# Optimization experiments

Measured on AMD Instinct MI355X. Metric: run time of the kernel, lower is better.

Reference implementation:

```python
import jax, jax.numpy as jnp
import numpy as np

C_EXP = 8.0  # fixed gate sharpness from the module (self.c = 8.0)

def setup_inputs() -> dict:
    key = jax.random.key(0)
    k1, k2, k3, k4 = jax.random.split(key, 4)
    B, T, D = 8, 4096, 1024
    x = jax.random.normal(k1, (B, T, D), dtype=jnp.float32)
    W_r = jax.random.normal(k2, (D, D), dtype=jnp.float32) * (1.0 / np.sqrt(D))
    W_i = jax.random.normal(k3, (D, D), dtype=jnp.float32) * (1.0 / np.sqrt(D))
    lambd = jax.random.normal(k4, (D,), dtype=jnp.float32)
    return {"x": x, "W_r": W_r, "W_i": W_i, "lambd": lambd}

def reference(x, W_r, W_i, lambd):
    # Gates (nn.Linear with bias=False: y = x @ W.T)
    r = jax.nn.sigmoid(jnp.einsum('btd,ed->bte', x, W_r))
    i = jax.nn.sigmoid(jnp.einsum('btd,ed->bte', x, W_i))
    # a = sigmoid(lambd) ** (c * r), computed stably in log space
    log_a = C_EXP * r * jax.nn.log_sigmoid(lambd)  # [B,T,D], log_a <= 0
    a = jnp.exp(log_a)
    # input-normalized injection: sqrt(1 - a^2) * (i * x)
    b = jnp.sqrt(jnp.maximum(1.0 - jnp.exp(2.0 * log_a), 0.0)) * (i * x)
    # linear recurrence h_t = a_t * h_{t-1} + b_t via associative scan over T
    def combine(c1, c2):
        a1, b1 = c1
        a2, b2 = c2
        return (a1 * a2, a2 * b1 + b2)
    _, h = jax.lax.associative_scan(combine, (a, b), axis=1)
    return h
```

## Files before the change

### kernel.cpp

```cpp
#include <hip/hip_runtime.h>
#include <hip/hip_bf16.h>
#include <cstdint>

#define B_   8
#define T_   4096
#define D_   1024
#define M_   (B_*T_)
#define K_   D_
#define N_   D_

#define TC2  64
#define NC2  (T_/TC2)

#define BM   256
#define BN   128
#define BK   64
#define NSTEP (K_/BK)

typedef __attribute__((ext_vector_type(8))) short  short8;
typedef __attribute__((ext_vector_type(4))) float  floatx4;

#define XB_OFF    0ull
#define WR_OFF    (XB_OFF + (size_t)M_*K_*2)
#define WI_OFF    (WR_OFF + (size_t)N_*K_*2)
#define LS_OFF    (WI_OFF + (size_t)N_*K_*2)
#define ASUM_OFF  (LS_OFF + (size_t)D_*4)
#define ESUM_OFF  (ASUM_OFF + (size_t)B_*NC2*D_*4)
#define WS_NEED   (ESUM_OFF + (size_t)B_*NC2*D_*4)

__device__ __forceinline__ uint32_t f2bf(float f) {
  uint32_t u = __float_as_uint(f);
  return (u + 0x7fffu + ((u >> 16) & 1u)) >> 16;
}

__device__ __forceinline__ void gload_lds16(const void* g, void* l) {
  __builtin_amdgcn_global_load_lds(
      (const __attribute__((address_space(1))) void*)g,
      (__attribute__((address_space(3))) void*)l, 16, 0, 0);
}

__global__ __launch_bounds__(256) void convert_kernel(
    const float* __restrict__ x, const float* __restrict__ wr,
    const float* __restrict__ wi, const float* __restrict__ lambd,
    uint2* __restrict__ xb, uint2* __restrict__ wrb, uint2* __restrict__ wib,
    float* __restrict__ ls) {
  int gid = blockIdx.x * 256 + threadIdx.x;
  if (gid < D_) {
    float l = lambd[gid];
    ls[gid] = fminf(l, 0.f) - log1pf(__expf(-fabsf(l)));
  }
  const int XQ = M_*K_/4;
  const int WQ = N_*K_/4;
  int stride = gridDim.x * 256;
  for (int q = gid; q < XQ + 2*WQ; q += stride) {
    const float4* src; uint2* dst; int i;
    if (q < XQ)           { src = (const float4*)x;  dst = xb;  i = q; }
    else if (q < XQ + WQ) { src = (const float4*)wr; dst = wrb; i = q - XQ; }
    else                  { src = (const float4*)wi; dst = wib; i = q - XQ - WQ; }
    float4 v = src[i];
    uint2 o;
    o.x = (f2bf(v.y) << 16) | f2bf(v.x);
    o.y = (f2bf(v.w) << 16) | f2bf(v.z);
    dst[i] = o;
  }
}

__global__ __launch_bounds__(512, 2) void dual_gemm_kernel(
    const short* __restrict__ xb, const short* __restrict__ wrb,
    const short* __restrict__ wib, const float* __restrict__ ls,
    uint32_t* __restrict__ ab, float* __restrict__ Asum,
    float* __restrict__ Esum) {
  __shared__ short lds[2 * 32768];

  const int tid  = threadIdx.x;
  const int lane = tid & 63;
  const int wv   = tid >> 6;
  const int wm   = wv >> 1;
  const int wn   = wv & 1;
  const int c16  = lane & 15;
  const int q    = lane >> 4;

  const int bm = blockIdx.x * BM;
  const int bn = blockIdx.y * BN;

  floatx4 accR[4][4], accI[4][4];
  #pragma unroll
  for (int i = 0; i < 4; ++i)
    #pragma unroll
    for (int j = 0; j < 4; ++j) {
      accR[i][j] = (floatx4){0.f,0.f,0.f,0.f};
      accI[i][j] = (floatx4){0.f,0.f,0.f,0.f};
    }

  const int srow   = lane >> 3;
  const int schunk = lane & 7;

  auto stage = [&](int buf, int k0) {
    short* dst = lds + buf * 32768;
    #pragma unroll
    for (int l = 0; l < 4; ++l) {
      int r  = wv*32 + l*8 + srow;
      int cc = schunk ^ (r & 7);
      gload_lds16(xb + (size_t)(bm + r)*K_ + k0 + cc*8,
                  dst + wv*2048 + l*512);
    }
    #pragma unroll
    for (int l = 0; l < 2; ++l) {
      int r  = wv*16 + l*8 + srow;
      int cc = schunk ^ (r & 7);
      gload_lds16(wrb + (size_t)(bn + r)*K_ + k0 + cc*8,
                  dst + 16384 + wv*1024 + l*512);
      gload_lds16(wib + (size_t)(bn + r)*K_ + k0 + cc*8,
                  dst + 24576 + wv*1024 + l*512);
    }
  };

  stage(0, 0);
  __syncthreads();

  for (int step = 0; step < NSTEP; ++step) {
    if (step + 1 < NSTEP) stage((step + 1) & 1, (step + 1) * BK);

    const short* As  = lds + (step & 1) * 32768;
    const short* Brs = As + 16384;
    const short* Bis = As + 24576;

    #pragma unroll
    for (int kk = 0; kk < BK/32; ++kk) {
      short8 af[4], brf[4], bif[4];
      #pragma unroll
      for (int f = 0; f < 4; ++f) {
        int m_loc = wm*64 + f*16 + c16;
        int cph   = (kk*4 + q) ^ (m_loc & 7);
        af[f]  = *(const short8*)(As  + m_loc*64 + cph*8);
        int n_loc = wn*64 + f*16 + c16;
        int cphn  = (kk*4 + q) ^ (n_loc & 7);
        brf[f] = *(const short8*)(Brs + n_loc*64 + cphn*8);
        bif[f] = *(const short8*)(Bis + n_loc*64 + cphn*8);
      }
      __builtin_amdgcn_s_setprio(1);
      #pragma unroll
      for (int fm = 0; fm < 4; ++fm)
        #pragma unroll
        for (int fn = 0; fn < 4; ++fn) {
          accR[fm][fn] = __builtin_amdgcn_mfma_f32_16x16x32_bf16(
              af[fm], brf[fn], accR[fm][fn], 0, 0, 0);
          accI[fm][fn] = __builtin_amdgcn_mfma_f32_16x16x32_bf16(
              af[fm], bif[fn], accI[fm][fn], 0, 0, 0);
        }
      __builtin_amdgcn_s_setprio(0);
    }
    __syncthreads();
  }

  const int b_idx = bm >> 12;
  const int c2    = ((bm & (T_-1)) >> 6) + wm;
  #pragma unroll
  for (int fn = 0; fn < 4; ++fn) {
    int col = bn + wn*64 + fn*16 + c16;
    float lsv = ls[col];
    float WA = 1.f, WE = 0.f;
    #pragma unroll
    for (int fm = 0; fm < 4; ++fm) {
      float SA = 1.f, SE = 0.f;
      #pragma unroll
      for (int j = 0; j < 4; ++j) {
        int row = bm + wm*64 + fm*16 + q*4 + j;
        float pr = accR[fm][fn][j];
        float pi = accI[fm][fn][j];
        float rg = 1.f / (1.f + __expf(-pr));
        float ig = 1.f / (1.f + __expf(-pi));
        float la = 8.f * rg * lsv;
        uint32_t xu = (uint32_t)(uint16_t)xb[(size_t)row*K_ + col];
        float xv = __uint_as_float(xu << 16);
        float a2 = __expf(2.f * la);
        float bb = sqrtf(fmaxf(1.f - a2, 0.f)) * ig * xv;
        uint32_t pk = (f2bf(bb) << 16) | f2bf(la);
        ab[(size_t)row*N_ + col] = pk;
        float av  = __expf(__uint_as_float(pk << 16));
        float bbr = __uint_as_float(pk & 0xffff0000u);
        SA *= av;
        SE = fmaf(av, SE, bbr);
      }
      #pragma unroll
      for (int s = 16; s <= 32; s <<= 1) {
        float OA = __shfl_xor(SA, s);
        float OE = __shfl_xor(SE, s);
        SE = (lane & s) ? fmaf(SA, OE, SE)
                        : fmaf(OA, SE, OE);
        SA *= OA;
      }
      WE = fmaf(SA, WE, SE);
      WA *= SA;
    }
    if (q == 0) {
      int o = (b_idx * NC2 + c2) * D_ + col;
      Asum[o] = WA;
      Esum[o] = WE;
    }
  }
}

__global__ __launch_bounds__(256) void scan_carry(
    float* __restrict__ Asum, const float* __restrict__ Esum) {
  int b = blockIdx.x >> 2;
  int d = ((blockIdx.x & 3) << 8) + threadIdx.x;
  float carry = 0.f;
  #pragma unroll 8
  for (int c = 0; c < NC2; ++c) {
    int o = (b*NC2 + c)*D_ + d;
    float A = Asum[o], E = Esum[o];
    Asum[o] = carry;
    carry = fmaf(A, carry, E);
  }
}

__global__ __launch_bounds__(256) void scan_final(
    uint32_t* __restrict__ out, const float* __restrict__ carry_buf) {
  int blk = blockIdx.x;
  int dg = blk & 1;
  int c  = (blk >> 1) & (NC2 - 1);
  int b  = blk >> 7;
  int d2 = (dg << 8) + threadIdx.x;

  const float2* cb = (const float2*)(carry_buf + (size_t)(b*NC2 + c)*D_);
  float2 hc = cb[d2];
  float h0 = hc.x, h1 = hc.y;

  uint2* p = (uint2*)(out + ((size_t)(b*T_ + c*TC2))*D_) + d2;
  #pragma unroll 4
  for (int t = 0; t < TC2; ++t) {
    size_t o = (size_t)t * (D_/2);
    uint2 v = p[o];
    float a0 = __expf(__uint_as_float(v.x << 16));
    h0 = fmaf(a0, h0, __uint_as_float(v.x & 0xffff0000u));
    float a1 = __expf(__uint_as_float(v.y << 16));
    h1 = fmaf(a1, h1, __uint_as_float(v.y & 0xffff0000u));
    uint2 ov; ov.x = __float_as_uint(h0); ov.y = __float_as_uint(h1);
    p[o] = ov;
  }
}

extern "C" void kernel_launch(void* const* d_in, const int* in_sizes, int n_in,
                              void* d_out, int out_size, void* d_ws, size_t ws_size,
                              hipStream_t stream) {
  (void)in_sizes; (void)n_in; (void)out_size;
  if (ws_size < WS_NEED) return;

  const float* x     = (const float*)d_in[0];
  const float* Wr    = (const float*)d_in[1];
  const float* Wi    = (const float*)d_in[2];
  const float* lambd = (const float*)d_in[3];

  char* ws = (char*)d_ws;
  short* xb   = (short*)(ws + XB_OFF);
  short* wrb  = (short*)(ws + WR_OFF);
  short* wib  = (short*)(ws + WI_OFF);
  float* ls   = (float*)(ws + LS_OFF);
  float* Asum = (float*)(ws + ASUM_OFF);
  float* Esum = (float*)(ws + ESUM_OFF);

  uint32_t* ab = (uint32_t*)d_out;

  convert_kernel<<<4096, 256, 0, stream>>>(x, Wr, Wi, lambd,
                                           (uint2*)xb, (uint2*)wrb, (uint2*)wib, ls);
  dual_gemm_kernel<<<dim3(M_/BM, N_/BN), 512, 0, stream>>>(xb, wrb, wib, ls, ab,
                                                           Asum, Esum);
  scan_carry<<<B_ * 4, 256, 0, stream>>>(Asum, Esum);
  scan_final<<<B_ * NC2 * 2, 256, 0, stream>>>(ab, Asum);
}
```

Baseline: 439.6 us.

## Interleave split global-to-LDS staging with MFMA clusters in dual GEMM main loop

Breaks each K-step into four phases, each loading one fragment set from LDS, issuing one slice of the next tile's global-to-LDS prefetch, then running a 16-MFMA cluster between raw s_barriers. Explicit vmcnt waits replace __syncthreads so loads stay in flight across phases. The goal is to spread memory traffic across the compute window and keep the matrix units busy, in the style of ping-pong scheduling. The cost is more barriers per step and correctness that depends on the hand-counted vmcnt values.

Measured after the change: 453.5 us. +3.2%, slower.

```diff
diff --git a/kernel.cpp b/kernel.cpp
--- a/kernel.cpp
+++ b/kernel.cpp
@@ -38,6 +38,14 @@
       (const __attribute__((address_space(1))) void*)g,
       (__attribute__((address_space(3))) void*)l, 16, 0, 0);
 }
+
+#define MFMA_CLUSTER(ACC, AF, BF)                                        \
+  _Pragma("unroll")                                                      \
+  for (int fm = 0; fm < 4; ++fm)                                         \
+    _Pragma("unroll")                                                    \
+    for (int fn = 0; fn < 4; ++fn)                                       \
+      ACC[fm][fn] = __builtin_amdgcn_mfma_f32_16x16x32_bf16(             \
+          AF[fm], BF[fn], ACC[fm][fn], 0, 0, 0);
 
 __global__ __launch_bounds__(256) void convert_kernel(
     const float* __restrict__ x, const float* __restrict__ wr,
@@ -95,62 +103,97 @@
   const int srow   = lane >> 3;
   const int schunk = lane & 7;
 
-  auto stage = [&](int buf, int k0) {
+  auto stageA = [&](int buf, int k0, int half) {
     short* dst = lds + buf * 32768;
     #pragma unroll
-    for (int l = 0; l < 4; ++l) {
+    for (int i = 0; i < 2; ++i) {
+      int l  = half*2 + i;
       int r  = wv*32 + l*8 + srow;
       int cc = schunk ^ (r & 7);
       gload_lds16(xb + (size_t)(bm + r)*K_ + k0 + cc*8,
                   dst + wv*2048 + l*512);
     }
+  };
+  auto stageB = [&](int buf, int k0, const short* W, int base) {
+    short* dst = lds + buf * 32768 + base;
     #pragma unroll
     for (int l = 0; l < 2; ++l) {
       int r  = wv*16 + l*8 + srow;
       int cc = schunk ^ (r & 7);
-      gload_lds16(wrb + (size_t)(bn + r)*K_ + k0 + cc*8,
-                  dst + 16384 + wv*1024 + l*512);
-      gload_lds16(wib + (size_t)(bn + r)*K_ + k0 + cc*8,
-                  dst + 24576 + wv*1024 + l*512);
+      gload_lds16(W + (size_t)(bn + r)*K_ + k0 + cc*8,
+                  dst + wv*1024 + l*512);
     }
   };
 
-  stage(0, 0);
-  __syncthreads();
+  stageA(0, 0, 0); stageA(0, 0, 1);
+  stageB(0, 0, wrb, 16384); stageB(0, 0, wib, 24576);
+  asm volatile("s_waitcnt vmcnt(2)" ::: "memory");
+  __builtin_amdgcn_s_barrier();
 
   for (int step = 0; step < NSTEP; ++step) {
-    if (step + 1 < NSTEP) stage((step + 1) & 1, (step + 1) * BK);
-
     const short* As  = lds + (step & 1) * 32768;
     const short* Brs = As + 16384;
     const short* Bis = As + 24576;
-
-    #pragma unroll
-    for (int kk = 0; kk < BK/32; ++kk) {
-      short8 af[4], brf[4], bif[4];
-      #pragma unroll
-      for (int f = 0; f < 4; ++f) {
-        int m_loc = wm*64 + f*16 + c16;
-        int cph   = (kk*4 + q) ^ (m_loc & 7);
-        af[f]  = *(const short8*)(As  + m_loc*64 + cph*8);
-        int n_loc = wn*64 + f*16 + c16;
-        int cphn  = (kk*4 + q) ^ (n_loc & 7);
-        brf[f] = *(const short8*)(Brs + n_loc*64 + cphn*8);
-        bif[f] = *(const short8*)(Bis + n_loc*64 + cphn*8);
-      }
-      __builtin_amdgcn_s_setprio(1);
-      #pragma unroll
-      for (int fm = 0; fm < 4; ++fm)
-        #pragma unroll
-        for (int fn = 0; fn < 4; ++fn) {
-          accR[fm][fn] = __builtin_amdgcn_mfma_f32_16x16x32_bf16(
-              af[fm], brf[fn], accR[fm][fn], 0, 0, 0);
-          accI[fm][fn] = __builtin_amdgcn_mfma_f32_16x16x32_bf16(
-              af[fm], bif[fn], accI[fm][fn], 0, 0, 0);
-        }
-      __builtin_amdgcn_s_setprio(0);
-    }
-    __syncthreads();
+    const int  nb  = (step + 1) & 1;
+    const int  nk  = (step + 1) * BK;
+    const bool pre = (step + 1 < NSTEP);
+
+    short8 af0[4], af1[4], bf[4];
+
+    #pragma unroll
+    for (int f = 0; f < 4; ++f) {
+      int m_loc = wm*64 + f*16 + c16;
+      af0[f] = *(const short8*)(As  + m_loc*64 + ((q) ^ (m_loc & 7))*8);
+      int n_loc = wn*64 + f*16 + c16;
+      bf[f]  = *(const short8*)(Brs + n_loc*64 + ((q) ^ (n_loc & 7))*8);
+    }
+    if (pre) stageA(nb, nk, 0);
+    __builtin_amdgcn_s_barrier();
+    __builtin_amdgcn_s_setprio(1);
+    MFMA_CLUSTER(accR, af0, bf);
+    __builtin_amdgcn_s_setprio(0);
+    if (pre) asm volatile("s_waitcnt vmcnt(2)" ::: "memory");
+    else     asm volatile("s_waitcnt vmcnt(0)" ::: "memory");
+    __builtin_amdgcn_s_barrier();
+
+    #pragma unroll
+    for (int f = 0; f < 4; ++f) {
+      int n_loc = wn*64 + f*16 + c16;
+      bf[f] = *(const short8*)(Bis + n_loc*64 + ((q) ^ (n_loc & 7))*8);
+    }
+    if (pre) stageA(nb, nk, 1);
+    __builtin_amdgcn_s_barrier();
+    __builtin_amdgcn_s_setprio(1);
+    MFMA_CLUSTER(accI, af0, bf);
+    __builtin_amdgcn_s_setprio(0);
+    __builtin_amdgcn_s_barrier();
+
+    #pragma unroll
+    for (int f = 0; f < 4; ++f) {
+      int m_loc = wm*64 + f*16 + c16;
+      af1[f] = *(const short8*)(As  + m_loc*64 + ((4 + q) ^ (m_loc & 7))*8);
+      int n_loc = wn*64 + f*16 + c16;
+      bf[f]  = *(const short8*)(Brs + n_loc*64 + ((4 + q) ^ (n_loc & 7))*8);
+    }
+    if (pre) stageB(nb, nk, wrb, 16384);
+    __builtin_amdgcn_s_barrier();
+    __builtin_amdgcn_s_setprio(1);
+    MFMA_CLUSTER(accR, af1, bf);
+    __builtin_amdgcn_s_setprio(0);
+    __builtin_amdgcn_s_barrier();
+
+    #pragma unroll
+    for (int f = 0; f < 4; ++f) {
+      int n_loc = wn*64 + f*16 + c16;
+      bf[f] = *(const short8*)(Bis + n_loc*64 + ((4 + q) ^ (n_loc & 7))*8);
+    }
+    if (pre) stageB(nb, nk, wib, 24576);
+    __builtin_amdgcn_s_barrier();
+    __builtin_amdgcn_s_setprio(1);
+    MFMA_CLUSTER(accI, af1, bf);
+    __builtin_amdgcn_s_setprio(0);
+    if (pre) asm volatile("s_waitcnt vmcnt(2)" ::: "memory");
+    __builtin_amdgcn_s_barrier();
   }
 
   const int b_idx = bm >> 12;
```
